# Optimization experiments

Measured on AMD Instinct MI355X. Metric: run time of the kernel, lower is better.

The kernel has to match this reference:

```python
import jax, jax.numpy as jnp
import numpy as np

N, E, T, F, HID, NCLS = 50000, 800000, 6, 64, 48, 2
LN_EPS = 1e-5


def setup_inputs() -> dict:
    key = jax.random.key(0)
    ks = jax.random.split(key, 24)
    p = lambda k, shape, s=0.1: jax.random.normal(k, shape, dtype=jnp.float32) * s
    inp = {
        "x_seq": jax.random.normal(ks[0], (T, N, F), dtype=jnp.float32),
        "edge_index": jax.random.randint(ks[1], (2, E), 0, N, dtype=jnp.int64),
        "edge_weight": jax.random.uniform(ks[2], (E,), dtype=jnp.float32),
        # GCN layer 0
        "W0": p(ks[3], (F, HID)), "b0": jnp.zeros((HID,), jnp.float32),
        "g0": jnp.ones((HID,), jnp.float32), "be0": jnp.zeros((HID,), jnp.float32),
        # GCN layer 1
        "W1": p(ks[4], (HID, HID)), "b1": jnp.zeros((HID,), jnp.float32),
        "g1": jnp.ones((HID,), jnp.float32), "be1": jnp.zeros((HID,), jnp.float32),
        # GRU (torch gate order: r, z, n)
        "W_ih": p(ks[5], (3 * HID, HID)), "W_hh": p(ks[6], (3 * HID, HID)),
        "b_ih": jnp.zeros((3 * HID,), jnp.float32), "b_hh": jnp.zeros((3 * HID,), jnp.float32),
        # classifier MLP
        "Wc1": p(ks[7], (HID, HID // 2)), "bc1": jnp.zeros((HID // 2,), jnp.float32),
        "Wc2": p(ks[8], (HID // 2, NCLS)), "bc2": jnp.zeros((NCLS,), jnp.float32),
    }
    return inp


def _layer_norm(x, g, b):
    mu = x.mean(-1, keepdims=True)
    var = ((x - mu) ** 2).mean(-1, keepdims=True)
    return (x - mu) * jax.lax.rsqrt(var + LN_EPS) * g + b


def reference(x_seq, edge_index, edge_weight, W0, b0, g0, be0, W1, b1, g1, be1,
              W_ih, W_hh, b_ih, b_hh, Wc1, bc1, Wc2, bc2):
    n = x_seq.shape[1]
    hid = W0.shape[1]
    row, col = edge_index[0], edge_index[1]
    # PyG GCNConv default: add self-loops (weight 1), symmetric normalization
    loop = jnp.arange(n)
    row_f = jnp.concatenate([row, loop])
    col_f = jnp.concatenate([col, loop])
    w_f = jnp.concatenate([edge_weight, jnp.ones((n,), edge_weight.dtype)])
    deg = jax.ops.segment_sum(w_f, col_f, num_segments=n)
    dis = jnp.where(deg > 0, jax.lax.rsqrt(jnp.maximum(deg, 1e-12)), 0.0)
    norm = dis[row_f] * w_f * dis[col_f]  # [E+N]

    def gcn(x, W, b):
        h = x @ W                              # [N, hid]
        msg = h[row_f] * norm[:, None]         # [E+N, hid]
        return jax.ops.segment_sum(msg, col_f, num_segments=n) + b

    def spatial(x_t):
        # layer 0: no residual (in_dim != hid)
        h1 = jax.nn.relu(_layer_norm(gcn(x_t, W0, b0), g0, be0))
        # layer 1: residual (dropout is eval-mode no-op)
        h2 = jax.nn.relu(_layer_norm(gcn(h1, W1, b1), g1, be1)) + h1
        return h2

    # sequential map over T keeps per-step [E,hid] message buffers small
    H = jax.lax.map(spatial, x_seq)            # [T, N, hid]

    def gru_step(h, x_t):
        gi = x_t @ W_ih.T + b_ih               # [N, 3*hid]
        gh = h @ W_hh.T + b_hh
        i_r, i_z, i_n = jnp.split(gi, 3, axis=-1)
        h_r, h_z, h_n = jnp.split(gh, 3, axis=-1)
        r = jax.nn.sigmoid(i_r + h_r)
        z = jax.nn.sigmoid(i_z + h_z)
        nv = jnp.tanh(i_n + r * h_n)
        h_new = (1.0 - z) * nv + z * h
        return h_new, None

    h0 = jnp.zeros((n, hid), x_seq.dtype)
    z_last, _ = jax.lax.scan(gru_step, h0, H)  # last hidden state [N, hid]

    logits = jax.nn.relu(z_last @ Wc1 + bc1) @ Wc2 + bc2  # [N, 2]
    return logits
```

## Files before the change

### kernel.cpp

```cpp
#include <hip/hip_runtime.h>
#include <math.h>

#define NN 50000
#define NE 800000
#define TT 6
#define HID 48
#define NB 196
#define LR 65

typedef unsigned short ushortT;

__device__ __forceinline__ float sigmoidf_(float x){ return 1.0f/(1.0f+__expf(-x)); }
__device__ __forceinline__ float tanhf_(float x){
  float xc = fminf(fmaxf(x,-15.f),15.f);
  float t = __expf(2.f*xc);
  return (t-1.f)/(t+1.f);
}
__device__ __forceinline__ unsigned f2bf(float x){
  unsigned u = __float_as_uint(x);
  return (u + 0x7fffu + ((u>>16)&1u)) >> 16;
}
__device__ __forceinline__ unsigned pack2(float a, float b){
  return f2bf(a) | (f2bf(b)<<16);
}
__device__ __forceinline__ float bflo(unsigned u){ return __uint_as_float(u<<16); }
__device__ __forceinline__ float bfhi(unsigned u){ return __uint_as_float(u & 0xffff0000u); }
__device__ __forceinline__ float bfu(ushortT u){ return __uint_as_float(((unsigned)u)<<16); }

struct U3 { unsigned x,y,z; };

__device__ __forceinline__ int block_scan_incl(int x, int* wsum){
  int lane = threadIdx.x & 63, w = threadIdx.x >> 6;
  int v = x;
#pragma unroll
  for(int d=1; d<64; d<<=1){
    int u = __shfl_up(v, d, 64);
    if(lane >= d) v += u;
  }
  if(lane==63) wsum[w] = v;
  __syncthreads();
  int add = 0;
#pragma unroll
  for(int k=0;k<3;k++) if(w>k) add += wsum[k];
  return v + add;
}

__global__ __launch_bounds__(256) void k_setup(int* cnt,
                                               const float* __restrict__ Wih, const float* __restrict__ Whh,
                                               float* Wp, float* Wgh){
  int i = blockIdx.x*256+threadIdx.x;
  if(i<NN) cnt[i]=0;
  if(i < 6912){
    int g = i/2304, rem = i%2304;
    int k = rem/48, f = rem%48;
    Wp[i] = Wih[(g*48+f)*48 + k];
  } else if(i < 13824){
    int idx = i-6912;
    int wv = idx/1152, rem = idx%1152;
    int k = rem/24, m = rem%24;
    int g = m>>3, j = m&7;
    Wgh[idx] = Whh[(g*48+wv*8+j)*48 + k];
  }
}

__global__ __launch_bounds__(256) void k_cnt(const int* __restrict__ ei, int* cnt, int* pos){
  int e = blockIdx.x*256+threadIdx.x;
  if(e<NE){
    int c = ei[NE+e];
    pos[e] = atomicAdd(&cnt[c], 1);
  }
}

__global__ __launch_bounds__(256) void k_partA(const int* __restrict__ cnt, int* bsum){
  __shared__ int wsum[4];
  int i = blockIdx.x*256+threadIdx.x;
  int x = (i<NN)? cnt[i] : 0;
  int lane = threadIdx.x & 63, w = threadIdx.x >> 6;
  int v = x;
#pragma unroll
  for(int m=32;m>=1;m>>=1) v += __shfl_xor(v, m, 64);
  if(lane==0) wsum[w]=v;
  __syncthreads();
  if(threadIdx.x==0) bsum[blockIdx.x] = wsum[0]+wsum[1]+wsum[2]+wsum[3];
}

__global__ __launch_bounds__(256) void k_midB(const int* __restrict__ bsum, int* bpre, int* offs){
  __shared__ int wsum[4];
  int t = threadIdx.x;
  int x = (t<NB)? bsum[t] : 0;
  int incl = block_scan_incl(x, wsum);
  if(t<NB) bpre[t] = incl - x;
  if(t==255) offs[NN] = incl;
}

__global__ __launch_bounds__(256) void k_offsC(const int* __restrict__ cnt, const int* __restrict__ bpre,
                                               int* offs){
  __shared__ int wsum[4];
  int i = blockIdx.x*256+threadIdx.x;
  int x = (i<NN)? cnt[i] : 0;
  int incl = block_scan_incl(x, wsum);
  if(i<NN) offs[i] = bpre[blockIdx.x] + incl - x;
}

__global__ __launch_bounds__(256) void k_scatter(const int* __restrict__ ei, const float* __restrict__ ew,
                                                 const int* __restrict__ offs, const int* __restrict__ pos,
                                                 int2* __restrict__ csr){
  int e = blockIdx.x*256+threadIdx.x;
  if(e<NE){
    int c = ei[NE+e];
    int2 v; v.x = ei[e]; v.y = __float_as_int(ew[e]);
    csr[offs[c]+pos[e]] = v;
  }
}

__global__ __launch_bounds__(256) void k_deg(const int2* __restrict__ csr, const int* __restrict__ offs,
                                             float* dis){
  int i = blockIdx.x*256+threadIdx.x;
  if(i<NN){
    float s = 1.f;
    int e0=offs[i], e1=offs[i+1];
    for(int j=e0;j<e1;j++) s += __int_as_float(csr[j].y);
    dis[i] = rsqrtf(s);
  }
}

__global__ __launch_bounds__(256) void k_normE(int2* __restrict__ csr, const float* __restrict__ dis){
  int j = blockIdx.x*256+threadIdx.x;
  if(j<NE){
    int2 v = csr[j];
    v.y = __float_as_int(dis[v.x]*__int_as_float(v.y));
    csr[j] = v;
  }
}

__global__ __launch_bounds__(256) void k_mm0(const float* __restrict__ X, const float* __restrict__ W,
                                             unsigned* __restrict__ A){
  int s = __builtin_amdgcn_readfirstlane(threadIdx.x>>6);
  int n = blockIdx.x*64 + (threadIdx.x&63);
  if(n>=NN) return;
  const float* xb = X + (long long)n*64;
  const float* wb = W + 12*s;
  float acc[TT][12];
#pragma unroll
  for(int t=0;t<TT;t++)
#pragma unroll
    for(int j=0;j<12;j++) acc[t][j]=0.f;
#pragma unroll 2
  for(int k4=0;k4<16;k4++){
    float4 xv[TT];
#pragma unroll
    for(int t=0;t<TT;t++) xv[t] = *reinterpret_cast<const float4*>(xb + (long long)t*NN*64 + 4*k4);
#pragma unroll
    for(int q=0;q<4;q++){
      const float* wr = wb + (4*k4+q)*HID;
      float w[12];
#pragma unroll
      for(int j=0;j<12;j++) w[j]=wr[j];
#pragma unroll
      for(int t=0;t<TT;t++){
        float xs = (&xv[t].x)[q];
#pragma unroll
        for(int j=0;j<12;j++) acc[t][j] = fmaf(xs, w[j], acc[t][j]);
      }
    }
  }
  unsigned buf[36];
#pragma unroll
  for(int j=0;j<12;j++){
    buf[3*j  ]=pack2(acc[0][j],acc[1][j]);
    buf[3*j+1]=pack2(acc[2][j],acc[3][j]);
    buf[3*j+2]=pack2(acc[4][j],acc[5][j]);
  }
  uint4* o4 = reinterpret_cast<uint4*>(A + (long long)n*144 + 36*s);
#pragma unroll
  for(int q=0;q<9;q++) o4[q] = make_uint4(buf[4*q],buf[4*q+1],buf[4*q+2],buf[4*q+3]);
}

__global__ __launch_bounds__(256) void k_mm1(const float* __restrict__ X, const float* __restrict__ W,
                                             unsigned* __restrict__ A){
  int s = __builtin_amdgcn_readfirstlane(threadIdx.x>>6);
  int n = blockIdx.x*64 + (threadIdx.x&63);
  if(n>=NN) return;
  const float* xb = X + (long long)n*(TT*HID);
  const float* wb = W + 12*s;
  float acc[TT][12];
#pragma unroll
  for(int t=0;t<TT;t++)
#pragma unroll
    for(int j=0;j<12;j++) acc[t][j]=0.f;
#pragma unroll 2
  for(int k4=0;k4<12;k4++){
    float4 xv[TT];
#pragma unroll
    for(int t=0;t<TT;t++) xv[t] = *reinterpret_cast<const float4*>(xb + t*HID + 4*k4);
#pragma unroll
    for(int q=0;q<4;q++){
      const float* wr = wb + (4*k4+q)*HID;
      float w[12];
#pragma unroll
      for(int j=0;j<12;j++) w[j]=wr[j];
#pragma unroll
      for(int t=0;t<TT;t++){
        float xs = (&xv[t].x)[q];
#pragma unroll
        for(int j=0;j<12;j++) acc[t][j] = fmaf(xs, w[j], acc[t][j]);
      }
    }
  }
  unsigned buf[36];
#pragma unroll
  for(int j=0;j<12;j++){
    buf[3*j  ]=pack2(acc[0][j],acc[1][j]);
    buf[3*j+1]=pack2(acc[2][j],acc[3][j]);
    buf[3*j+2]=pack2(acc[4][j],acc[5][j]);
  }
  uint4* o4 = reinterpret_cast<uint4*>(A + (long long)n*144 + 36*s);
#pragma unroll
  for(int q=0;q<9;q++) o4[q] = make_uint4(buf[4*q],buf[4*q+1],buf[4*q+2],buf[4*q+3]);
}

__global__ __launch_bounds__(256) void k_agg(const unsigned* __restrict__ A, const float* __restrict__ bias,
                                             const float* __restrict__ gain, const float* __restrict__ beta,
                                             const float* __restrict__ resid, float* __restrict__ out,
                                             const int* __restrict__ offs, const int2* __restrict__ csr,
                                             const float* __restrict__ dis){
  int wid = (blockIdx.x*256+threadIdx.x)>>6;
  int lane = threadIdx.x & 63;
  if(wid>=NN) return;
  const bool act = lane<HID;
  const int f = act? lane : (HID-1);
  float dn = dis[wid];
  float acc[TT];
  {
    U3 v = *reinterpret_cast<const U3*>(A + (long long)wid*144 + 3*f);
    acc[0]=dn*bflo(v.x); acc[1]=dn*bfhi(v.x);
    acc[2]=dn*bflo(v.y); acc[3]=dn*bfhi(v.y);
    acc[4]=dn*bflo(v.z); acc[5]=dn*bfhi(v.z);
  }
  int e0=offs[wid], e1=offs[wid+1];
  int e=e0;
  for(; e+3<e1; e+=4){
    int2 i0=csr[e], i1=csr[e+1], i2=csr[e+2], i3=csr[e+3];
    U3 d0 = *reinterpret_cast<const U3*>(A + (long long)i0.x*144 + 3*f);
    U3 d1 = *reinterpret_cast<const U3*>(A + (long long)i1.x*144 + 3*f);
    U3 d2 = *reinterpret_cast<const U3*>(A + (long long)i2.x*144 + 3*f);
    U3 d3 = *reinterpret_cast<const U3*>(A + (long long)i3.x*144 + 3*f);
    float n0=__int_as_float(i0.y), n1=__int_as_float(i1.y);
    float n2=__int_as_float(i2.y), n3=__int_as_float(i3.y);
    acc[0]=fmaf(n0,bflo(d0.x),acc[0]); acc[1]=fmaf(n0,bfhi(d0.x),acc[1]);
    acc[2]=fmaf(n0,bflo(d0.y),acc[2]); acc[3]=fmaf(n0,bfhi(d0.y),acc[3]);
    acc[4]=fmaf(n0,bflo(d0.z),acc[4]); acc[5]=fmaf(n0,bfhi(d0.z),acc[5]);
    acc[0]=fmaf(n1,bflo(d1.x),acc[0]); acc[1]=fmaf(n1,bfhi(d1.x),acc[1]);
    acc[2]=fmaf(n1,bflo(d1.y),acc[2]); acc[3]=fmaf(n1,bfhi(d1.y),acc[3]);
    acc[4]=fmaf(n1,bflo(d1.z),acc[4]); acc[5]=fmaf(n1,bfhi(d1.z),acc[5]);
    acc[0]=fmaf(n2,bflo(d2.x),acc[0]); acc[1]=fmaf(n2,bfhi(d2.x),acc[1]);
    acc[2]=fmaf(n2,bflo(d2.y),acc[2]); acc[3]=fmaf(n2,bfhi(d2.y),acc[3]);
    acc[4]=fmaf(n2,bflo(d2.z),acc[4]); acc[5]=fmaf(n2,bfhi(d2.z),acc[5]);
    acc[0]=fmaf(n3,bflo(d3.x),acc[0]); acc[1]=fmaf(n3,bfhi(d3.x),acc[1]);
    acc[2]=fmaf(n3,bflo(d3.y),acc[2]); acc[3]=fmaf(n3,bfhi(d3.y),acc[3]);
    acc[4]=fmaf(n3,bflo(d3.z),acc[4]); acc[5]=fmaf(n3,bfhi(d3.z),acc[5]);
  }
  for(; e<e1; ++e){
    int2 i0=csr[e];
    U3 d0 = *reinterpret_cast<const U3*>(A + (long long)i0.x*144 + 3*f);
    float n0=__int_as_float(i0.y);
    acc[0]=fmaf(n0,bflo(d0.x),acc[0]); acc[1]=fmaf(n0,bfhi(d0.x),acc[1]);
    acc[2]=fmaf(n0,bflo(d0.y),acc[2]); acc[3]=fmaf(n0,bfhi(d0.y),acc[3]);
    acc[4]=fmaf(n0,bflo(d0.z),acc[4]); acc[5]=fmaf(n0,bfhi(d0.z),acc[5]);
  }
  float bb = bias[f], gg = gain[f], be = beta[f];
  const float rn = 1.0f/HID;
#pragma unroll
  for(int t=0;t<TT;t++){
    float val = fmaf(acc[t], dn, bb);
    float v = act? val : 0.f;
    float s = v, s2 = v*v;
#pragma unroll
    for(int m=32;m>=1;m>>=1){
      s  += __shfl_xor(s,  m, 64);
      s2 += __shfl_xor(s2, m, 64);
    }
    float mu  = s*rn;
    float var = fmaxf(s2*rn - mu*mu, 0.f);
    float y = (val-mu)*rsqrtf(var+1e-5f)*gg + be;
    y = fmaxf(y, 0.f);
    long long oidx = (long long)wid*(TT*HID) + t*HID + f;
    if(resid) y += resid[oidx];
    if(act) out[oidx] = y;
  }
}

__global__ __launch_bounds__(256) void k_mmG(const float* __restrict__ h2, const float* __restrict__ Wp,
                                             const float* __restrict__ bih, ushortT* __restrict__ gi){
  int g = blockIdx.x, t = blockIdx.y;
  int n = blockIdx.z*256 + threadIdx.x;
  if(n>=NN) return;
  const float* xr = h2 + (size_t)n*(TT*HID) + t*HID;
  const float* wb = Wp + g*2304;
  const float* bb = bih + g*48;
  float acc[48];
#pragma unroll
  for(int j=0;j<48;j++) acc[j]=bb[j];
#pragma unroll 2
  for(int k4=0;k4<12;k4++){
    float4 xv = *reinterpret_cast<const float4*>(xr + 4*k4);
#pragma unroll
    for(int q=0;q<4;q++){
      const float* wr = wb + (4*k4+q)*48;
      float w[48];
#pragma unroll
      for(int j=0;j<48;j++) w[j]=wr[j];
      float xs = (&xv.x)[q];
#pragma unroll
      for(int j=0;j<48;j++) acc[j] = fmaf(xs, w[j], acc[j]);
    }
  }
  size_t base = ((size_t)t*144 + g*48)*NN + n;
#pragma unroll
  for(int j=0;j<48;j++) gi[base + (size_t)j*NN] = (ushortT)f2bf(acc[j]);
}

__global__ __launch_bounds__(384) void k_gruF(const ushortT* __restrict__ gi,
                                              const float* __restrict__ Wgh,
                                              const float* __restrict__ bhh,
                                              const float* __restrict__ Wc1, const float* __restrict__ bc1,
                                              const float* __restrict__ Wc2, const float* __restrict__ bc2,
                                              float* __restrict__ out){
  __shared__ float hbuf[48*LR];
  int tid = threadIdx.x;
  int wv = __builtin_amdgcn_readfirstlane(tid>>6);
  int lane = tid & 63;
  int f0 = wv*8;
  long long nbase = (long long)blockIdx.x*64;

  for(int i=tid;i<48*LR;i+=384) hbuf[i]=0.f;

  float bhr[8], bhz[8], bhn[8];
#pragma unroll
  for(int j=0;j<8;j++){
    int f=f0+j;
    bhr[j] = bhh[f];
    bhz[j] = bhh[48+f];
    bhn[j] = bhh[96+f];
  }

  for(int t=0;t<TT;t++){
    float gr[8], gz[8], gn_[8];
    {
      const ushortT* gp = gi + ((size_t)t*144 + f0)*NN + nbase + lane;
#pragma unroll
      for(int j=0;j<8;j++){
        gr[j]  = bfu(gp[(size_t)j*NN]);
        gz[j]  = bfu(gp[(size_t)(48+j)*NN]);
        gn_[j] = bfu(gp[(size_t)(96+j)*NN]);
      }
    }
    __syncthreads();

    float ar[8],az[8],an[8];
#pragma unroll
    for(int j=0;j<8;j++){ ar[j]=az[j]=an[j]=0.f; }

#pragma unroll 4
    for(int k=0;k<48;k++){
      const float* wp = Wgh + (wv*48 + k)*24;
      float ws[24];
#pragma unroll
      for(int q=0;q<24;q++) ws[q]=wp[q];
      float hk = hbuf[k*LR+lane];
#pragma unroll
      for(int j=0;j<8;j++){
        ar[j]=fmaf(hk,ws[j],   ar[j]);
        az[j]=fmaf(hk,ws[8+j], az[j]);
        an[j]=fmaf(hk,ws[16+j],an[j]);
      }
    }

    float hn[8];
#pragma unroll
    for(int j=0;j<8;j++){
      float r  = sigmoidf_(gr[j] + ar[j] + bhr[j]);
      float zg = sigmoidf_(gz[j] + az[j] + bhz[j]);
      float ng = tanhf_(gn_[j] + r*(an[j] + bhn[j]));
      hn[j] = (1.f-zg)*ng + zg*hbuf[(f0+j)*LR+lane];
    }
    __syncthreads();
#pragma unroll
    for(int j=0;j<8;j++) hbuf[(f0+j)*LR+lane] = hn[j];
  }
  __syncthreads();

  if(wv==0){
    long long gn = nbase + lane;
    if(gn<NN){
      float hv[24];
#pragma unroll
      for(int j=0;j<24;j++) hv[j]=bc1[j];
      for(int k=0;k<HID;k++){
        float xk = hbuf[k*LR+lane];
        const float* wr = Wc1 + k*24;
#pragma unroll
        for(int j=0;j<24;j++) hv[j] = fmaf(xk, wr[j], hv[j]);
      }
      float l0=bc2[0], l1=bc2[1];
#pragma unroll
      for(int j=0;j<24;j++){
        float a = fmaxf(hv[j],0.f);
        l0 = fmaf(a, Wc2[2*j],   l0);
        l1 = fmaf(a, Wc2[2*j+1], l1);
      }
      reinterpret_cast<float2*>(out)[gn] = make_float2(l0,l1);
    }
  }
}

static inline size_t al256(size_t x){ return (x+255)&~(size_t)255; }

extern "C" void kernel_launch(void* const* d_in, const int* in_sizes, int n_in,
                              void* d_out, int out_size, void* d_ws, size_t ws_size,
                              hipStream_t stream){
  const float* x_seq=(const float*)d_in[0];
  const int*   ei   =(const int*)d_in[1];
  const float* ew   =(const float*)d_in[2];
  const float* W0=(const float*)d_in[3];  const float* b0=(const float*)d_in[4];
  const float* g0=(const float*)d_in[5];  const float* be0=(const float*)d_in[6];
  const float* W1=(const float*)d_in[7];  const float* b1=(const float*)d_in[8];
  const float* g1=(const float*)d_in[9];  const float* be1=(const float*)d_in[10];
  const float* Wih=(const float*)d_in[11];const float* Whh=(const float*)d_in[12];
  const float* bih=(const float*)d_in[13];const float* bhh=(const float*)d_in[14];
  const float* Wc1=(const float*)d_in[15];const float* bc1=(const float*)d_in[16];
  const float* Wc2=(const float*)d_in[17];const float* bc2=(const float*)d_in[18];
  float* outp=(float*)d_out;

  char* p=(char*)d_ws; size_t off=0;
  auto alloc=[&](size_t bytes)->void*{ void* r=p+off; off=al256(off+bytes); return r; };
  float* dis    =(float*)alloc((size_t)NN*4);
  int*   cnt    =(int*)  alloc((size_t)NN*4);
  int*   offs   =(int*)  alloc((size_t)(NN+1)*4);
  int*   bsum   =(int*)  alloc((size_t)NB*4);
  int*   bpre   =(int*)  alloc((size_t)NB*4);
  int*   pos    =(int*)  alloc((size_t)NE*4);
  int2*  csr    =(int2*) alloc((size_t)NE*8);
  float* Wp     =(float*)alloc((size_t)3*48*48*4);
  float* Wgh    =(float*)alloc((size_t)6*48*24*4);
  unsigned* A   =(unsigned*)alloc((size_t)NN*576 + 1024);
  float* h1     =(float*)alloc((size_t)NN*TT*HID*4);
  float* h2     =(float*)alloc((size_t)NN*TT*HID*4);
  ushortT* gi   =(ushortT*)A;

  const int GN=(NN+255)/256, GE=(NE+255)/256;
  const int GMM=(NN+63)/64;
  const int GAGG=(NN*64+255)/256;
  const int GGRU=(NN+63)/64;

  k_setup  <<<GN,256,0,stream>>>(cnt,Wih,Whh,Wp,Wgh);
  k_cnt    <<<GE,256,0,stream>>>(ei,cnt,pos);
  k_partA  <<<NB,256,0,stream>>>(cnt,bsum);
  k_midB   <<<1,256,0,stream>>>(bsum,bpre,offs);
  k_offsC  <<<NB,256,0,stream>>>(cnt,bpre,offs);
  k_scatter<<<GE,256,0,stream>>>(ei,ew,offs,pos,csr);
  k_deg    <<<GN,256,0,stream>>>(csr,offs,dis);
  k_normE  <<<GE,256,0,stream>>>(csr,dis);

  k_mm0<<<GMM,256,0,stream>>>(x_seq, W0, A);
  k_agg<<<GAGG,256,0,stream>>>(A,b0,g0,be0,nullptr,h1,offs,csr,dis);
  k_mm1<<<GMM,256,0,stream>>>(h1, W1, A);
  k_agg<<<GAGG,256,0,stream>>>(A,b1,g1,be1,h1,h2,offs,csr,dis);
  k_mmG<<<dim3(3,6,NB),256,0,stream>>>(h2, Wp, bih, gi);
  k_gruF<<<GGRU,384,0,stream>>>(gi, Wgh, bhh, Wc1,bc1,Wc2,bc2, outp);
}
```

Before: 727.8 us.

## Stage GRU input and weight tiles in LDS for gate matmuls

The input-gate matmul kernel now uses 768-thread blocks that cooperatively load a 256-node tile of h2 and all three gate weight blocks into shared memory. Each wave group computes one gate from LDS, so the three gates share one set of global loads and uncoalesced per-thread row reads become coalesced float4 loads. The GRU recurrence kernel also copies its hidden-to-hidden weights into LDS and reads them with float4 loads instead of scalar global loads. The cost is much more LDS per block (about 77KB for the matmul kernel), which can limit occupancy.

```diff
diff --git a/kernel.cpp b/kernel.cpp
--- a/kernel.cpp
+++ b/kernel.cpp
@@ -290,34 +290,50 @@
   }
 }
 
-__global__ __launch_bounds__(256) void k_mmG(const float* __restrict__ h2, const float* __restrict__ Wp,
+__global__ __launch_bounds__(768) void k_mmG(const float* __restrict__ h2, const float* __restrict__ Wp,
                                              const float* __restrict__ bih, ushortT* __restrict__ gi){
-  int g = blockIdx.x, t = blockIdx.y;
-  int n = blockIdx.z*256 + threadIdx.x;
-  if(n>=NN) return;
-  const float* xr = h2 + (size_t)n*(TT*HID) + t*HID;
-  const float* wb = Wp + g*2304;
+  __shared__ float xb[256*49];
+  __shared__ float wb[3*48*48];
+  int tid = threadIdx.x;
+  int t = blockIdx.x;
+  long long nbase = (long long)blockIdx.y*256;
+  for(int i=tid;i<6912;i+=768) wb[i]=Wp[i];
+#pragma unroll
+  for(int i=0;i<4;i++){
+    int c = tid + 768*i;
+    int nd = c/12, fc = c-12*nd;
+    long long gn = nbase+nd; if(gn>NN-1) gn=NN-1;
+    float4 v = *reinterpret_cast<const float4*>(h2 + gn*(TT*HID) + t*HID + fc*4);
+    float* d = xb + nd*49 + fc*4;
+    d[0]=v.x; d[1]=v.y; d[2]=v.z; d[3]=v.w;
+  }
+  __syncthreads();
+  int g = __builtin_amdgcn_readfirstlane(tid>>8);
+  int nd = tid & 255;
   const float* bb = bih + g*48;
   float acc[48];
 #pragma unroll
   for(int j=0;j<48;j++) acc[j]=bb[j];
+  const float* wg = wb + g*2304;
 #pragma unroll 2
-  for(int k4=0;k4<12;k4++){
-    float4 xv = *reinterpret_cast<const float4*>(xr + 4*k4);
-#pragma unroll
-    for(int q=0;q<4;q++){
-      const float* wr = wb + (4*k4+q)*48;
-      float w[48];
-#pragma unroll
-      for(int j=0;j<48;j++) w[j]=wr[j];
-      float xs = (&xv.x)[q];
-#pragma unroll
-      for(int j=0;j<48;j++) acc[j] = fmaf(xs, w[j], acc[j]);
-    }
-  }
-  size_t base = ((size_t)t*144 + g*48)*NN + n;
-#pragma unroll
-  for(int j=0;j<48;j++) gi[base + (size_t)j*NN] = (ushortT)f2bf(acc[j]);
+  for(int k=0;k<48;k++){
+    float xk = xb[nd*49+k];
+    const float* wr = wg + k*48;
+#pragma unroll
+    for(int j4=0;j4<12;j4++){
+      float4 w = *reinterpret_cast<const float4*>(wr + 4*j4);
+      acc[4*j4  ] = fmaf(xk, w.x, acc[4*j4  ]);
+      acc[4*j4+1] = fmaf(xk, w.y, acc[4*j4+1]);
+      acc[4*j4+2] = fmaf(xk, w.z, acc[4*j4+2]);
+      acc[4*j4+3] = fmaf(xk, w.w, acc[4*j4+3]);
+    }
+  }
+  long long n = nbase + nd;
+  if(n<NN){
+    size_t base = ((size_t)t*144 + g*48)*NN + n;
+#pragma unroll
+    for(int j=0;j<48;j++) gi[base + (size_t)j*NN] = (ushortT)f2bf(acc[j]);
+  }
 }
 
 __global__ __launch_bounds__(384) void k_gruF(const ushortT* __restrict__ gi,
@@ -327,6 +343,7 @@
                                               const float* __restrict__ Wc2, const float* __restrict__ bc2,
                                               float* __restrict__ out){
   __shared__ float hbuf[48*LR];
+  __shared__ float wlds[6*48*24];
   int tid = threadIdx.x;
   int wv = __builtin_amdgcn_readfirstlane(tid>>6);
   int lane = tid & 63;
@@ -334,6 +351,7 @@
   long long nbase = (long long)blockIdx.x*64;
 
   for(int i=tid;i<48*LR;i+=384) hbuf[i]=0.f;
+  for(int i=tid;i<6912;i+=384) wlds[i]=Wgh[i];
 
   float bhr[8], bhz[8], bhn[8];
 #pragma unroll
@@ -363,16 +381,19 @@
 
 #pragma unroll 4
     for(int k=0;k<48;k++){
-      const float* wp = Wgh + (wv*48 + k)*24;
-      float ws[24];
-#pragma unroll
-      for(int q=0;q<24;q++) ws[q]=wp[q];
+      const float* wp = wlds + (wv*48 + k)*24;
       float hk = hbuf[k*LR+lane];
-#pragma unroll
-      for(int j=0;j<8;j++){
-        ar[j]=fmaf(hk,ws[j],   ar[j]);
-        az[j]=fmaf(hk,ws[8+j], az[j]);
-        an[j]=fmaf(hk,ws[16+j],an[j]);
+      float4 w0=*reinterpret_cast<const float4*>(wp);
+      float4 w1=*reinterpret_cast<const float4*>(wp+4);
+      float4 w2=*reinterpret_cast<const float4*>(wp+8);
+      float4 w3=*reinterpret_cast<const float4*>(wp+12);
+      float4 w4=*reinterpret_cast<const float4*>(wp+16);
+      float4 w5=*reinterpret_cast<const float4*>(wp+20);
+#pragma unroll
+      for(int c=0;c<4;c++){
+        ar[c]  =fmaf(hk,(&w0.x)[c],ar[c]);   ar[4+c]=fmaf(hk,(&w1.x)[c],ar[4+c]);
+        az[c]  =fmaf(hk,(&w2.x)[c],az[c]);   az[4+c]=fmaf(hk,(&w3.x)[c],az[4+c]);
+        an[c]  =fmaf(hk,(&w4.x)[c],an[c]);   an[4+c]=fmaf(hk,(&w5.x)[c],an[4+c]);
       }
     }
 
@@ -466,6 +487,6 @@
   k_agg<<<GAGG,256,0,stream>>>(A,b0,g0,be0,nullptr,h1,offs,csr,dis);
   k_mm1<<<GMM,256,0,stream>>>(h1, W1, A);
   k_agg<<<GAGG,256,0,stream>>>(A,b1,g1,be1,h1,h2,offs,csr,dis);
-  k_mmG<<<dim3(3,6,NB),256,0,stream>>>(h2, Wp, bih, gi);
+  k_mmG<<<dim3(TT,NB),768,0,stream>>>(h2, Wp, bih, gi);
   k_gruF<<<GGRU,384,0,stream>>>(gi, Wgh, bhh, Wc1,bc1,Wc2,bc2, outp);
 }
```

Measured after the change: 770.2 us. 1.06x slower.
